# Optimization experiments

Hardware: AMD Instinct MI355X
Metric: run time of the kernel (lower is better)

## Reference

```python
import jax, jax.numpy as jnp
import numpy as np

D_MODEL = 1024
N_HEAD = 16
D_HEAD = D_MODEL // N_HEAD


def setup_inputs() -> dict:
    key = jax.random.key(0)
    ks = jax.random.split(key, 12)
    L, B, M = 2048, 2, 2048
    s = 1.0 / np.sqrt(D_MODEL)
    return {
        "q": jax.random.normal(ks[0], (L, B, D_MODEL), jnp.float32),
        "kv": jax.random.normal(ks[1], (L, B, D_MODEL), jnp.float32),
        "mem": jax.random.normal(ks[2], (M, B, D_MODEL), jnp.float32),
        "w_q": jax.random.normal(ks[3], (D_MODEL, D_MODEL), jnp.float32) * s,
        "b_q": jnp.zeros((D_MODEL,), jnp.float32),
        "w_k": jax.random.normal(ks[4], (D_MODEL, D_MODEL), jnp.float32) * s,
        "b_k": jnp.zeros((D_MODEL,), jnp.float32),
        "w_v": jax.random.normal(ks[5], (D_MODEL, D_MODEL), jnp.float32) * s,
        "b_v": jnp.zeros((D_MODEL,), jnp.float32),
        "w_c": jax.random.normal(ks[6], (D_MODEL, D_MODEL), jnp.float32) * s,
        "b_c": jnp.zeros((D_MODEL,), jnp.float32),
    }


def reference(q, kv, mem, w_q, b_q, w_k, b_k, w_v, b_v, w_c, b_c):
    # c: [L+M, B, D]
    c = jnp.concatenate([mem, kv], axis=0)
    L, B, _ = q.shape
    J = c.shape[0]
    # linear projections (torch Linear: x @ W^T + b)
    qh = (q @ w_q.T + b_q).reshape(L, B, N_HEAD, D_HEAD)
    kh = (c @ w_k.T + b_k).reshape(J, B, N_HEAD, D_HEAD)
    vh = (c @ w_v.T + b_v).reshape(J, B, N_HEAD, D_HEAD)
    # attention scores [i, j, b, n]
    score = jnp.einsum("ibnd,jbnd->ijbn", qh, kh) / np.sqrt(D_HEAD).astype(np.float32)
    prob = jax.nn.softmax(score, axis=1)
    vec = jnp.einsum("ijbn,jbnd->ibnd", prob, vh).reshape(L, B, D_MODEL)
    return vec @ w_c.T + b_c
```

## Files before the change

kernel.cpp:

```cpp
#include <hip/hip_runtime.h>


using short8 = __attribute__((ext_vector_type(8))) short;
using f32x4  = __attribute__((ext_vector_type(4))) float;

#define DEV __device__ __forceinline__

DEV unsigned short f2bf(float f) {
  union { float f; unsigned int u; } x; x.f = f;
  unsigned int r = x.u + 0x7FFFu + ((x.u >> 16) & 1u);
  return (unsigned short)(r >> 16);
}

DEV unsigned int cvtpk(float lo, float hi) {
  unsigned int r;
  asm("v_cvt_pk_bf16_f32 %0, %1, %2" : "=v"(r) : "v"(lo), "v"(hi));
  return r;
}

DEV float max3f(float a, float b, float c) {
  float d;
  asm("v_max3_f32 %0, %1, %2, %3" : "=v"(d) : "v"(a), "v"(b), "v"(c));
  return d;
}

DEV void gload_lds16(const unsigned short* g, unsigned short* l) {
  __builtin_amdgcn_global_load_lds(
      (const __attribute__((address_space(1))) unsigned int*)g,
      (__attribute__((address_space(3))) unsigned int*)l, 16, 0, 0);
}

#define BARRIER_RAW()                      \
  do {                                     \
    __builtin_amdgcn_sched_barrier(0);     \
    __builtin_amdgcn_s_barrier();          \
    __builtin_amdgcn_sched_barrier(0);     \
  } while (0)

__global__ __launch_bounds__(256) void convert_all(
    const float* __restrict__ q, const float* __restrict__ mem_,
    const float* __restrict__ kv, const float* __restrict__ wq,
    const float* __restrict__ wk, const float* __restrict__ wv,
    const float* __restrict__ wc, unsigned short* __restrict__ a_bf,
    unsigned short* __restrict__ c_bf, unsigned short* __restrict__ w_bf) {
  size_t u = (size_t)blockIdx.x * 256 + threadIdx.x;
  const float* src;
  unsigned short* dst;
  if (u < 524288u)        { src = q    + u * 8;                dst = a_bf + u * 8; }
  else if (u < 1048576u)  { src = mem_ + (u - 524288u) * 8;    dst = c_bf + (u - 524288u) * 8; }
  else if (u < 1572864u)  { src = kv   + (u - 1048576u) * 8;   dst = c_bf + 4194304u + (u - 1048576u) * 8; }
  else if (u < 1703936u)  { src = wq   + (u - 1572864u) * 8;   dst = w_bf + (u - 1572864u) * 8; }
  else if (u < 1835008u)  { src = wk   + (u - 1703936u) * 8;   dst = w_bf + 1048576u + (u - 1703936u) * 8; }
  else if (u < 1966080u)  { src = wv   + (u - 1835008u) * 8;   dst = w_bf + 2097152u + (u - 1835008u) * 8; }
  else                    { src = wc   + (u - 1966080u) * 8;   dst = w_bf + 3145728u + (u - 1966080u) * 8; }
  float4 v0 = ((const float4*)src)[0];
  float4 v1 = ((const float4*)src)[1];
  union { unsigned short us[8]; uint4 v; } o;
  o.us[0] = f2bf(v0.x); o.us[1] = f2bf(v0.y); o.us[2] = f2bf(v0.z); o.us[3] = f2bf(v0.w);
  o.us[4] = f2bf(v1.x); o.us[5] = f2bf(v1.y); o.us[6] = f2bf(v1.z); o.us[7] = f2bf(v1.w);
  *(uint4*)dst = o.v;
}

__global__ __launch_bounds__(256, 2) void gemm_out(
    const unsigned short* __restrict__ A, const unsigned short* __restrict__ Bw,
    const float* __restrict__ bias, float* __restrict__ outp) {
  __shared__ __align__(16) unsigned short lA[64 * 64];
  __shared__ __align__(16) unsigned short lB[128 * 64];
  const int tid = threadIdx.x;
  const int lane = tid & 63;
  const int w = tid >> 6;
  const int wr = w >> 1, wcn = w & 1;
  const int tm = blockIdx.x * 64;
  const int tn = blockIdx.y * 128;

  const int srow = lane >> 3;
  const int scol = ((lane & 7) ^ srow) * 8;
  const unsigned short* aptr = A + (size_t)(tm + 16 * w + srow) * 1024 + scol;
  const unsigned short* bptr = Bw + (size_t)(tn + 32 * w + srow) * 1024 + scol;
  unsigned short* lAw = &lA[(16 * w) * 64];
  unsigned short* lBw = &lB[(32 * w) * 64];

  const f32x4 zero = {0.f, 0.f, 0.f, 0.f};
  f32x4 acc[2][4];
#pragma unroll
  for (int i = 0; i < 2; ++i)
#pragma unroll
    for (int j = 0; j < 4; ++j) acc[i][j] = zero;

  for (int kb = 0; kb < 16; ++kb) {
    const int ko = kb * 64;
#pragma unroll
    for (int c = 0; c < 2; ++c)
      gload_lds16(aptr + ko + c * 8 * 1024, lAw + c * 8 * 64);
#pragma unroll
    for (int c = 0; c < 4; ++c)
      gload_lds16(bptr + ko + c * 8 * 1024, lBw + c * 8 * 64);
    __syncthreads();
#pragma unroll
    for (int kk = 0; kk < 2; ++kk) {
      short8 af[2], bfr[4];
#pragma unroll
      for (int mi = 0; mi < 2; ++mi) {
        int r = 32 * wr + 16 * mi + (lane & 15);
        int slot = (kk * 4 + (lane >> 4)) ^ (r & 7);
        af[mi] = *(const short8*)&lA[r * 64 + slot * 8];
      }
#pragma unroll
      for (int ni = 0; ni < 4; ++ni) {
        int r = 64 * wcn + 16 * ni + (lane & 15);
        int slot = (kk * 4 + (lane >> 4)) ^ (r & 7);
        bfr[ni] = *(const short8*)&lB[r * 64 + slot * 8];
      }
#pragma unroll
      for (int mi = 0; mi < 2; ++mi)
#pragma unroll
        for (int ni = 0; ni < 4; ++ni)
          acc[mi][ni] = __builtin_amdgcn_mfma_f32_16x16x32_bf16(
              af[mi], bfr[ni], acc[mi][ni], 0, 0, 0);
    }
    __syncthreads();
  }

  const int g4 = (lane >> 4) * 4;
  const int c0 = lane & 15;
#pragma unroll
  for (int mi = 0; mi < 2; ++mi) {
#pragma unroll
    for (int ni = 0; ni < 4; ++ni) {
      const int colt = tn + 64 * wcn + 16 * ni + c0;
      const float bv = bias[colt];
#pragma unroll
      for (int j = 0; j < 4; ++j) {
        const int rowt = tm + 32 * wr + 16 * mi + g4 + j;
        outp[(size_t)rowt * 1024 + colt] = acc[mi][ni][j] + bv;
      }
    }
  }
}

__global__ __launch_bounds__(256, 2) void gemm_proj(
    const unsigned short* __restrict__ a_bf, const unsigned short* __restrict__ c_bf,
    const unsigned short* __restrict__ w_bf, const float* __restrict__ bq,
    const float* __restrict__ bk, const float* __restrict__ bv,
    unsigned short* __restrict__ qh, unsigned short* __restrict__ kh,
    unsigned short* __restrict__ vt) {
  const int yy = blockIdx.y;
  const int mode = yy >> 3;
  if (mode == 2 && blockIdx.x >= 32) return;
  __shared__ __align__(16) unsigned short lA[128 * 64];
  __shared__ __align__(16) unsigned short lB[128 * 64];
  const int tid = threadIdx.x;
  const int lane = tid & 63;
  const int w = tid >> 6;
  const int wr = w >> 1, wcn = w & 1;
  const int tm = blockIdx.x * 128;
  const int tn = (yy & 7) * 128;
  const unsigned short* A  = (mode == 2) ? a_bf : c_bf;
  const unsigned short* Bw = (mode == 0) ? w_bf + (1u << 20)
                            : (mode == 1) ? w_bf + (2u << 20) : w_bf;
  const float* bias = (mode == 0) ? bk : (mode == 1) ? bv : bq;

  const int srow = lane >> 3;
  const int scol = ((lane & 7) ^ srow) * 8;
  const unsigned short* aptr = A + (size_t)(tm + 32 * w + srow) * 1024 + scol;
  const unsigned short* bptr = Bw + (size_t)(tn + 32 * w + srow) * 1024 + scol;
  unsigned short* lAw = &lA[(32 * w) * 64];
  unsigned short* lBw = &lB[(32 * w) * 64];

  const f32x4 zero = {0.f, 0.f, 0.f, 0.f};
  f32x4 acc[4][4];
#pragma unroll
  for (int i = 0; i < 4; ++i)
#pragma unroll
    for (int j = 0; j < 4; ++j) acc[i][j] = zero;

  for (int kb = 0; kb < 16; ++kb) {
    const int ko = kb * 64;
#pragma unroll
    for (int c = 0; c < 4; ++c) {
      gload_lds16(aptr + ko + c * 8 * 1024, lAw + c * 8 * 64);
      gload_lds16(bptr + ko + c * 8 * 1024, lBw + c * 8 * 64);
    }
    __syncthreads();
#pragma unroll
    for (int kk = 0; kk < 2; ++kk) {
      short8 af[4], bfr[4];
#pragma unroll
      for (int mi = 0; mi < 4; ++mi) {
        int r = 64 * wr + 16 * mi + (lane & 15);
        int slot = (kk * 4 + (lane >> 4)) ^ (r & 7);
        af[mi] = *(const short8*)&lA[r * 64 + slot * 8];
      }
#pragma unroll
      for (int ni = 0; ni < 4; ++ni) {
        int r = 64 * wcn + 16 * ni + (lane & 15);
        int slot = (kk * 4 + (lane >> 4)) ^ (r & 7);
        bfr[ni] = *(const short8*)&lB[r * 64 + slot * 8];
      }
#pragma unroll
      for (int mi = 0; mi < 4; ++mi)
#pragma unroll
        for (int ni = 0; ni < 4; ++ni)
          acc[mi][ni] = __builtin_amdgcn_mfma_f32_16x16x32_bf16(
              af[mi], bfr[ni], acc[mi][ni], 0, 0, 0);
    }
    __syncthreads();
  }

  const int g4 = (lane >> 4) * 4;
  const int c0 = lane & 15;
#pragma unroll
  for (int mi = 0; mi < 4; ++mi) {
#pragma unroll
    for (int ni = 0; ni < 4; ++ni) {
      const int colt = tn + 64 * wcn + 16 * ni + c0;
      const float bvv = bias[colt];
#pragma unroll
      for (int j = 0; j < 4; ++j) {
        const int rowt = tm + 64 * wr + 16 * mi + g4 + j;
        const float v = acc[mi][ni][j] + bvv;
        const int jj = rowt >> 1, b = rowt & 1, n = colt >> 6, d = colt & 63;
        if (mode == 0) {
          kh[(((size_t)(b * 16 + n) * 4096 + jj) << 6) + d] = f2bf(v);
        } else if (mode == 1) {
          const int j6 = jj & 63;
          const int pos = (j6 & 3) | (((j6 >> 4) & 1) << 2) | (((j6 >> 2) & 3) << 3) |
                          (((j6 >> 5) & 1) << 5);
          vt[((size_t)(b * 16 + n) * 64 + d) * 4096 + (jj & ~63) + pos] = f2bf(v);
        } else {
          qh[(((size_t)(b * 16 + n) * 2048 + jj) << 6) + d] =
              f2bf(v * 0.1803368801111f);
        }
      }
    }
  }
}

__global__ __launch_bounds__(256, 2) void attn_kernel(
    const unsigned short* __restrict__ qh, const unsigned short* __restrict__ kh,
    const unsigned short* __restrict__ vt, unsigned short* __restrict__ vec) {
  __shared__ __align__(16) unsigned short kl[2][2][64 * 64];
  __shared__ __align__(16) unsigned short vl[2][2][64 * 64];
  const int tid = threadIdx.x;
  const int lane = tid & 63;
  const int w = tid >> 6;
  const int g = lane >> 4;
  const int l4 = lane & 15;
  const int f = blockIdx.x;
  const int head = (f & 7) * 4 + ((f >> 3) & 3);
  const int qt = f >> 5;
  const int b = head >> 4, n = head & 15;
  const unsigned short* qbase = qh + ((size_t)head * 2048 + qt * 128 + 32 * w) * 64;
  const unsigned short* kbase = kh + (size_t)head * 4096 * 64;
  const unsigned short* vbase = vt + (size_t)head * 64 * 4096;

  short8 qf[2][2];
#pragma unroll
  for (int mi = 0; mi < 2; ++mi)
#pragma unroll
    for (int kk = 0; kk < 2; ++kk)
      qf[mi][kk] = *(const short8*)&qbase[(16 * mi + l4) * 64 + kk * 32 + g * 8];

  const f32x4 zero = {0.f, 0.f, 0.f, 0.f};
  f32x4 oacc[2][4];
#pragma unroll
  for (int mi = 0; mi < 2; ++mi)
#pragma unroll
    for (int nd = 0; nd < 4; ++nd) oacc[mi][nd] = zero;
  float mrow[2] = {-3.0e38f, -3.0e38f};
  float lsum[2] = {0.f, 0.f};

  const int srow = lane >> 3;
  const int scol = ((lane & 7) ^ srow) * 8;
  const unsigned short* kp = kbase + (size_t)(16 * w + srow) * 64 + scol;
  const unsigned short* vp = vbase + (size_t)(16 * w + srow) * 4096 + scol;

  auto stage_pair = [&](int jp, int bufi) {
#pragma unroll
    for (int sub = 0; sub < 2; ++sub) {
      gload_lds16(kp + (size_t)jp * 8192 + sub * 4096,
                  &kl[bufi][sub][(16 * w) * 64]);
      gload_lds16(kp + (size_t)jp * 8192 + sub * 4096 + 8 * 64,
                  &kl[bufi][sub][(16 * w + 8) * 64]);
      gload_lds16(vp + jp * 128 + sub * 64, &vl[bufi][sub][(16 * w) * 64]);
      gload_lds16(vp + jp * 128 + sub * 64 + 8 * 4096,
                  &vl[bufi][sub][(16 * w + 8) * 64]);
    }
  };

  auto qkt = [&](const unsigned short* kbuf, f32x4 (&s)[2][4]) {
#pragma unroll
    for (int mi = 0; mi < 2; ++mi)
#pragma unroll
      for (int nj = 0; nj < 4; ++nj) s[mi][nj] = zero;
    __builtin_amdgcn_s_setprio(1);
#pragma unroll
    for (int kk = 0; kk < 2; ++kk) {
      short8 bk[4];
#pragma unroll
      for (int nj = 0; nj < 4; ++nj) {
        int r = 16 * nj + l4;
        int slot = (kk * 4 + g) ^ (r & 7);
        bk[nj] = *(const short8*)&kbuf[r * 64 + slot * 8];
      }
#pragma unroll
      for (int mi = 0; mi < 2; ++mi)
#pragma unroll
        for (int nj = 0; nj < 4; ++nj)
          s[mi][nj] = __builtin_amdgcn_mfma_f32_16x16x32_bf16(bk[nj], qf[mi][kk], s[mi][nj], 0, 0, 0);
    }
    __builtin_amdgcn_s_setprio(0);
  };

  auto sm = [&](f32x4 (&s)[2][4], short8 (&pa)[2][2]) {
    float pm[2];
#pragma unroll
    for (int mi = 0; mi < 2; ++mi) {
      float t0 = max3f(s[mi][0][0], s[mi][0][1], s[mi][0][2]);
      float t1 = max3f(s[mi][0][3], s[mi][1][0], s[mi][1][1]);
      float t2 = max3f(s[mi][1][2], s[mi][1][3], s[mi][2][0]);
      float t3 = max3f(s[mi][2][1], s[mi][2][2], s[mi][2][3]);
      float t4 = max3f(s[mi][3][0], s[mi][3][1], s[mi][3][2]);
      float p5 = max3f(t0, t1, t2);
      p5 = max3f(p5, t3, t4);
      pm[mi] = fmaxf(p5, s[mi][3][3]);
    }
    float pj = fmaxf(pm[0], pm[1]);
    pj = fmaxf(pj, __shfl_xor(pj, 16));
    pj = fmaxf(pj, __shfl_xor(pj, 32));
    if (!__all(pj <= fminf(mrow[0], mrow[1]) + 8.f)) {
#pragma unroll
      for (int mi = 0; mi < 2; ++mi) {
        const float mnew = fmaxf(mrow[mi], pj);
        const float sc = __builtin_amdgcn_exp2f(mrow[mi] - mnew);
        mrow[mi] = mnew;
        lsum[mi] *= sc;
#pragma unroll
        for (int reg = 0; reg < 4; ++reg) {
          const float scr = __shfl(sc, 4 * g + reg);
#pragma unroll
          for (int nd = 0; nd < 4; ++nd) oacc[mi][nd][reg] *= scr;
        }
      }
    }
#pragma unroll
    for (int mi = 0; mi < 2; ++mi) {
      const float m = mrow[mi];
      float tr[4];
#pragma unroll
      for (int nj = 0; nj < 4; ++nj) {
        const float p0 = __builtin_amdgcn_exp2f(s[mi][nj][0] - m);
        const float p1 = __builtin_amdgcn_exp2f(s[mi][nj][1] - m);
        const float p2 = __builtin_amdgcn_exp2f(s[mi][nj][2] - m);
        const float p3 = __builtin_amdgcn_exp2f(s[mi][nj][3] - m);
        s[mi][nj][0] = p0; s[mi][nj][1] = p1; s[mi][nj][2] = p2; s[mi][nj][3] = p3;
        tr[nj] = (p0 + p1) + (p2 + p3);
      }
      lsum[mi] += (tr[0] + tr[1]) + (tr[2] + tr[3]);
#pragma unroll
      for (int kk2 = 0; kk2 < 2; ++kk2) {
        union { unsigned int u[4]; short8 v; } t;
#pragma unroll
        for (int wd = 0; wd < 4; ++wd) {
          const int nj = (wd >> 1) + 2 * kk2;
          const int r0 = (wd & 1) * 2;
          t.u[wd] = cvtpk(s[mi][nj][r0], s[mi][nj][r0 + 1]);
        }
        pa[mi][kk2] = t.v;
      }
    }
  };

  auto pv = [&](const short8 (&pa)[2][2], const unsigned short* vbuf) {
    __builtin_amdgcn_s_setprio(1);
#pragma unroll
    for (int kk2 = 0; kk2 < 2; ++kk2) {
      short8 bv4[4];
#pragma unroll
      for (int nd = 0; nd < 4; ++nd) {
        const int r = 16 * nd + l4;
        const int blk = (g + 4 * kk2) ^ (r & 7);
        bv4[nd] = *(const short8*)&vbuf[r * 64 + blk * 8];
      }
#pragma unroll
      for (int mi = 0; mi < 2; ++mi)
#pragma unroll
        for (int nd = 0; nd < 4; ++nd)
          oacc[mi][nd] = __builtin_amdgcn_mfma_f32_16x16x32_bf16(pa[mi][kk2], bv4[nd], oacc[mi][nd], 0, 0, 0);
    }
    __builtin_amdgcn_s_setprio(0);
  };

  f32x4 sA[2][4], sB[2][4];
  short8 paA[2][2], paB[2][2];
  auto pair = [&](int bufi) {
    qkt(kl[bufi][0], sA);
    qkt(kl[bufi][1], sB);
    sm(sA, paA);
    pv(paA, vl[bufi][0]);
    sm(sB, paB);
    pv(paB, vl[bufi][1]);
  };

  stage_pair(0, 0);
  asm volatile("s_waitcnt vmcnt(0)" ::: "memory");
  BARRIER_RAW();

  for (int t2 = 0; t2 < 16; ++t2) {
    stage_pair(2 * t2 + 1, 1);
    pair(0);
    asm volatile("s_waitcnt vmcnt(0)" ::: "memory");
    BARRIER_RAW();
    if (t2 < 15) stage_pair(2 * t2 + 2, 0);
    pair(1);
    if (t2 < 15) {
      asm volatile("s_waitcnt vmcnt(0)" ::: "memory");
      BARRIER_RAW();
    }
  }

#pragma unroll
  for (int mi = 0; mi < 2; ++mi) {
    float l = lsum[mi];
    l += __shfl_xor(l, 16);
    l += __shfl_xor(l, 32);
#pragma unroll
    for (int reg = 0; reg < 4; ++reg) {
      const float lr = __shfl(l, 4 * g + reg);
      const float inv = 1.f / lr;
      const int i = qt * 128 + 32 * w + 16 * mi + 4 * g + reg;
#pragma unroll
      for (int nd = 0; nd < 4; ++nd) {
        const int d = 16 * nd + l4;
        vec[(size_t)(i * 2 + b) * 1024 + n * 64 + d] = f2bf(oacc[mi][nd][reg] * inv);
      }
    }
  }
}

extern "C" void kernel_launch(void* const* d_in, const int* in_sizes, int n_in,
                              void* d_out, int out_size, void* d_ws, size_t ws_size,
                              hipStream_t stream) {
  (void)in_sizes; (void)n_in; (void)out_size; (void)ws_size;
  const float* q    = (const float*)d_in[0];
  const float* kv   = (const float*)d_in[1];
  const float* mem_ = (const float*)d_in[2];
  const float* wq   = (const float*)d_in[3];
  const float* bq   = (const float*)d_in[4];
  const float* wk   = (const float*)d_in[5];
  const float* bk   = (const float*)d_in[6];
  const float* wv   = (const float*)d_in[7];
  const float* bv   = (const float*)d_in[8];
  const float* wc   = (const float*)d_in[9];
  const float* bc   = (const float*)d_in[10];

  char* ws = (char*)d_ws;
  unsigned short* w_bf = (unsigned short*)(ws);
  unsigned short* a_bf = (unsigned short*)(ws + (8ull << 20));
  unsigned short* c_bf = (unsigned short*)(ws + (16ull << 20));
  unsigned short* qhb  = (unsigned short*)(ws + (32ull << 20));
  unsigned short* khb  = (unsigned short*)(ws + (40ull << 20));
  unsigned short* vtb  = (unsigned short*)(ws + (56ull << 20));
  unsigned short* vecb = a_bf;

  convert_all<<<8192, 256, 0, stream>>>(q, mem_, kv, wq, wk, wv, wc, a_bf, c_bf, w_bf);
  gemm_proj<<<dim3(64, 24), 256, 0, stream>>>(a_bf, c_bf, w_bf, bq, bk, bv,
                                              qhb, khb, vtb);
  attn_kernel<<<512, 256, 0, stream>>>(qhb, khb, vtb, vecb);
  gemm_out<<<dim3(64, 8), 256, 0, stream>>>(vecb, w_bf + (3u << 20), bc, (float*)d_out);
}
```

Before: 174.6 us.

## Software-pipeline attention loop: overlap softmax with next tile's QK^T, triple-buffer V

```diff
diff --git a/kernel.cpp b/kernel.cpp
--- a/kernel.cpp
+++ b/kernel.cpp
@@ -240,7 +240,7 @@
     const unsigned short* __restrict__ qh, const unsigned short* __restrict__ kh,
     const unsigned short* __restrict__ vt, unsigned short* __restrict__ vec) {
   __shared__ __align__(16) unsigned short kl[2][2][64 * 64];
-  __shared__ __align__(16) unsigned short vl[2][2][64 * 64];
+  __shared__ __align__(16) unsigned short vl[3][2][64 * 64];
   const int tid = threadIdx.x;
   const int lane = tid & 63;
   const int w = tid >> 6;
@@ -275,16 +275,16 @@
   const unsigned short* kp = kbase + (size_t)(16 * w + srow) * 64 + scol;
   const unsigned short* vp = vbase + (size_t)(16 * w + srow) * 4096 + scol;
 
-  auto stage_pair = [&](int jp, int bufi) {
+  auto stage_pair = [&](int jp, int kb, int vb) {
 #pragma unroll
     for (int sub = 0; sub < 2; ++sub) {
       gload_lds16(kp + (size_t)jp * 8192 + sub * 4096,
-                  &kl[bufi][sub][(16 * w) * 64]);
+                  &kl[kb][sub][(16 * w) * 64]);
       gload_lds16(kp + (size_t)jp * 8192 + sub * 4096 + 8 * 64,
-                  &kl[bufi][sub][(16 * w + 8) * 64]);
-      gload_lds16(vp + jp * 128 + sub * 64, &vl[bufi][sub][(16 * w) * 64]);
+                  &kl[kb][sub][(16 * w + 8) * 64]);
+      gload_lds16(vp + jp * 128 + sub * 64, &vl[vb][sub][(16 * w) * 64]);
       gload_lds16(vp + jp * 128 + sub * 64 + 8 * 4096,
-                  &vl[bufi][sub][(16 * w + 8) * 64]);
+                  &vl[vb][sub][(16 * w + 8) * 64]);
     }
   };
 
@@ -391,33 +391,36 @@
     __builtin_amdgcn_s_setprio(0);
   };
 
-  f32x4 sA[2][4], sB[2][4];
-  short8 paA[2][2], paB[2][2];
-  auto pair = [&](int bufi) {
-    qkt(kl[bufi][0], sA);
-    qkt(kl[bufi][1], sB);
-    sm(sA, paA);
-    pv(paA, vl[bufi][0]);
-    sm(sB, paB);
-    pv(paB, vl[bufi][1]);
-  };
-
-  stage_pair(0, 0);
+  f32x4 s0[2][4], s1[2][4];
+  short8 pa0[2][2], pa1[2][2];
+
+  stage_pair(0, 0, 0);
   asm volatile("s_waitcnt vmcnt(0)" ::: "memory");
   BARRIER_RAW();
-
-  for (int t2 = 0; t2 < 16; ++t2) {
-    stage_pair(2 * t2 + 1, 1);
-    pair(0);
+  stage_pair(1, 1, 1);
+  qkt(kl[0][0], s0);
+  qkt(kl[0][1], s1);
+  asm volatile("s_waitcnt vmcnt(0)" ::: "memory");
+  BARRIER_RAW();
+
+  for (int p = 1; p < 32; ++p) {
+    const int kb = p & 1;
+    const int vb_prev = (p - 1) % 3;
+    if (p + 1 < 32) stage_pair(p + 1, (p + 1) & 1, (p + 1) % 3);
+    sm(s0, pa0);
+    sm(s1, pa1);
+    qkt(kl[kb][0], s0);
+    qkt(kl[kb][1], s1);
+    pv(pa0, vl[vb_prev][0]);
+    pv(pa1, vl[vb_prev][1]);
     asm volatile("s_waitcnt vmcnt(0)" ::: "memory");
     BARRIER_RAW();
-    if (t2 < 15) stage_pair(2 * t2 + 2, 0);
-    pair(1);
-    if (t2 < 15) {
-      asm volatile("s_waitcnt vmcnt(0)" ::: "memory");
-      BARRIER_RAW();
-    }
-  }
+  }
+
+  sm(s0, pa0);
+  sm(s1, pa1);
+  pv(pa0, vl[1][0]);
+  pv(pa1, vl[1][1]);
 
 #pragma unroll
   for (int mi = 0; mi < 2; ++mi) {
```

Measured after the change: 179.3 us. +2.7%, slower.
